# Kernel tuning notes

Hardware: AMD Instinct MI355X
Metric: run time of the kernel (lower is better)

Reference implementation:

```python
import jax, jax.numpy as jnp
import numpy as np
import math

D_MODEL = 1024
N_HEADS = 16
D_HEAD = 64
D_MLP = 4096
INIT_RANGE = 0.02
VAR_EPS = 1e-05
BATCH = 2
SEQ = 2048


def new_gelu(x):
    c = math.sqrt(2.0 / math.pi)
    return 0.5 * x * (1.0 + jnp.tanh(c * (x + 0.044715 * x ** 3)))


def layer_norm(x, w, b):
    mean = jnp.mean(x, axis=-1, keepdims=True)
    x = x - mean
    var = jnp.mean(x * x, axis=-1, keepdims=True)
    return x / jnp.sqrt(var + VAR_EPS) * w + b


def setup_inputs() -> dict:
    key = jax.random.key(0)
    ks = jax.random.split(key, 12)
    s = INIT_RANGE
    return {
        "resid": jax.random.normal(ks[0], (BATCH, SEQ, D_MODEL), jnp.float32),
        "w_q": s * jax.random.normal(ks[1], (N_HEADS, D_MODEL, D_HEAD), jnp.float32),
        "w_k": s * jax.random.normal(ks[2], (N_HEADS, D_MODEL, D_HEAD), jnp.float32),
        "w_v": s * jax.random.normal(ks[3], (N_HEADS, D_MODEL, D_HEAD), jnp.float32),
        "w_o": s * jax.random.normal(ks[4], (N_HEADS, D_HEAD, D_MODEL), jnp.float32),
        "ln1_w": s * jax.random.normal(ks[5], (D_MODEL,), jnp.float32),
        "ln1_b": jnp.zeros((D_MODEL,), jnp.float32),
        "ln2_w": s * jax.random.normal(ks[6], (D_MODEL,), jnp.float32),
        "ln2_b": jnp.zeros((D_MODEL,), jnp.float32),
        "w_in": s * jax.random.normal(ks[7], (D_MODEL, D_MLP), jnp.float32),
        "b_in": jnp.zeros((D_MLP,), jnp.float32),
        "w_out": s * jax.random.normal(ks[8], (D_MLP, D_MODEL), jnp.float32),
        "b_out": jnp.zeros((D_MODEL,), jnp.float32),
    }


def attention(x, w_q, w_k, w_v, w_o):
    # x: [b, s, d]; weights: [h, d, dh] / [h, dh, d]
    qs = jnp.einsum('bsd,hde->bhse', x, w_q)
    ks = jnp.einsum('bsd,hde->bhse', x, w_k)
    vs = jnp.einsum('bsd,hde->bhse', x, w_v)
    attn = jnp.einsum('bhqe,bhke->bhqk', qs, ks)  # [b, h, s, s]
    s = attn.shape[-1]
    causal = jnp.triu(jnp.ones((s, s), dtype=bool), k=1)
    attn = jnp.where(causal, -jnp.inf, attn)
    attn = jax.nn.softmax(attn / math.sqrt(D_HEAD), axis=-1)
    z = jnp.einsum('bhqk,bhke->bhqe', attn, vs)
    return jnp.einsum('bhse,hed->bsd', z, w_o)


def reference(resid, w_q, w_k, w_v, w_o, ln1_w, ln1_b, ln2_w, ln2_b, w_in, b_in, w_out, b_out):
    resid = resid + attention(layer_norm(resid, ln1_w, ln1_b), w_q, w_k, w_v, w_o)
    h = layer_norm(resid, ln2_w, ln2_b)
    h = new_gelu(jnp.einsum('bsd,dm->bsm', h, w_in) + b_in)
    resid = resid + jnp.einsum('bsm,md->bsd', h, w_out) + b_out
    return resid
```

## Files before the change

kernel.cpp:

```cpp
#include <hip/hip_runtime.h>

#define DEV static __device__ __forceinline__

typedef unsigned short u16;
typedef __attribute__((ext_vector_type(8))) __bf16 bf16x8;
typedef __attribute__((ext_vector_type(4))) float f32x4;

DEV float bf2f(u16 u) { union { unsigned int i; float f; } v; v.i = ((unsigned int)u) << 16; return v.f; }
DEV u16 f2bf(float f) {
  union { float f; unsigned int i; } v; v.f = f;
  unsigned int r = v.i + 0x7fffu + ((v.i >> 16) & 1u);
  return (u16)(r >> 16);
}

DEV float gelu_f(float x) {
  float u = 0.7978845608028654f * (x + 0.044715f * x * x * x);
  float e = __expf(2.f * u);
  float t = 1.f - 2.f / (e + 1.f);
  return 0.5f * x * (1.f + t);
}

DEV void async16(const u16* g, u16* l) {
  __builtin_amdgcn_global_load_lds(
      (const __attribute__((address_space(1))) unsigned int*)g,
      (__attribute__((address_space(3))) unsigned int*)l, 16, 0, 0);
}

__global__ __launch_bounds__(256) void transpose_conv(
    const float* __restrict__ in, u16* __restrict__ out, int R, int C,
    long inStride, long outStride)
{
  __shared__ float tile[32][33];
  const float* src = in + (size_t)blockIdx.z * inStride;
  u16* dst = out + (size_t)blockIdx.z * outStride;
  int c0 = blockIdx.x * 32, r0 = blockIdx.y * 32;
  int tx = threadIdx.x & 31, ty = threadIdx.x >> 5;
#pragma unroll
  for (int i = 0; i < 32; i += 8)
    tile[ty + i][tx] = src[(size_t)(r0 + ty + i) * C + (c0 + tx)];
  __syncthreads();
#pragma unroll
  for (int i = 0; i < 32; i += 8)
    dst[(size_t)(c0 + ty + i) * R + (r0 + tx)] = f2bf(tile[tx][ty + i]);
}

__global__ __launch_bounds__(256) void ln_kernel(
    const float* __restrict__ x, const float* __restrict__ g,
    const float* __restrict__ b, u16* __restrict__ out)
{
  int row = blockIdx.x, tid = threadIdx.x;
  const float4 v = ((const float4*)(x + (size_t)row * 1024))[tid];
  float s = v.x + v.y + v.z + v.w;
  float ss = v.x * v.x + v.y * v.y + v.z * v.z + v.w * v.w;
#pragma unroll
  for (int m = 1; m < 64; m <<= 1) { s += __shfl_xor(s, m, 64); ss += __shfl_xor(ss, m, 64); }
  __shared__ float red[8];
  if ((tid & 63) == 0) { red[tid >> 6] = s; red[4 + (tid >> 6)] = ss; }
  __syncthreads();
  s = red[0] + red[1] + red[2] + red[3];
  ss = red[4] + red[5] + red[6] + red[7];
  float mean = s * (1.f / 1024.f);
  float var = ss * (1.f / 1024.f) - mean * mean;
  float rstd = rsqrtf(var + 1e-5f);
  float4 gv = ((const float4*)g)[tid];
  float4 bv = ((const float4*)b)[tid];
  u16* o = out + (size_t)row * 1024 + tid * 4;
  o[0] = f2bf((v.x - mean) * rstd * gv.x + bv.x);
  o[1] = f2bf((v.y - mean) * rstd * gv.y + bv.y);
  o[2] = f2bf((v.z - mean) * rstd * gv.z + bv.z);
  o[3] = f2bf((v.w - mean) * rstd * gv.w + bv.w);
}

template <int EPI, int BM>
__global__ __launch_bounds__(256) void gemm_bf16(
    const u16* __restrict__ A, const u16* __restrict__ Bt, int K, int N,
    const float* __restrict__ addv, const float* __restrict__ bias,
    float* __restrict__ outF, u16* __restrict__ o0, u16* __restrict__ o1,
    u16* __restrict__ o2)
{
  constexpr int IT = BM / 32;
  __shared__ u16 lA[BM * 64];
  __shared__ u16 lB[128 * 64];
  const int tid = threadIdx.x;
  const int lane = tid & 63, wave = tid >> 6;
  const int wm = wave >> 1, wn = wave & 1;
  const int quad = lane >> 4, l16 = lane & 15;
  const int m0 = blockIdx.y * BM, n0 = blockIdx.x * 128;

  f32x4 acc[IT][4] = {};

  const int srow = lane >> 3;
  const int soff = ((lane & 7) ^ srow) << 3;

  for (int kt = 0; kt < K; kt += 64) {
    __syncthreads();
#pragma unroll
    for (int q = 0; q < BM / 32; ++q) {
      int rbase = wave * (BM / 4) + q * 8;
      async16(A + (size_t)(m0 + rbase + srow) * K + kt + soff, lA + rbase * 64);
    }
#pragma unroll
    for (int q = 0; q < 4; ++q) {
      int rbase = wave * 32 + q * 8;
      async16(Bt + (size_t)(n0 + rbase + srow) * K + kt + soff, lB + rbase * 64);
    }
    __syncthreads();
#pragma unroll
    for (int kk = 0; kk < 2; ++kk) {
      bf16x8 af[IT], bfr[4];
#pragma unroll
      for (int i = 0; i < IT; ++i) {
        int ar = wm * (BM / 2) + i * 16 + l16;
        af[i] = *(const bf16x8*)&lA[ar * 64 + ((((kk * 4) + quad) ^ (ar & 7)) << 3)];
      }
#pragma unroll
      for (int j = 0; j < 4; ++j) {
        int br = wn * 64 + j * 16 + l16;
        bfr[j] = *(const bf16x8*)&lB[br * 64 + ((((kk * 4) + quad) ^ (br & 7)) << 3)];
      }
#pragma unroll
      for (int i = 0; i < IT; ++i)
#pragma unroll
        for (int j = 0; j < 4; ++j)
          acc[i][j] = __builtin_amdgcn_mfma_f32_16x16x32_bf16(af[i], bfr[j], acc[i][j], 0, 0, 0);
    }
  }

#pragma unroll
  for (int i = 0; i < IT; ++i) {
    const int rowb = m0 + wm * (BM / 2) + i * 16 + quad * 4;
#pragma unroll
    for (int j = 0; j < 4; ++j) {
      const int col = n0 + wn * 64 + j * 16 + l16;
#pragma unroll
      for (int rr = 0; rr < 4; ++rr) {
        const int m = rowb + rr;
        const float v = acc[i][j][rr];
        if (EPI == 0) {
          int bb = m >> 11, s = m & 2047;
          int proj = col >> 10, hc = col & 1023, hh = hc >> 6, e = hc & 63;
          size_t bhh = (size_t)(bb * 16 + hh);
          if (proj == 0) o0[(bhh * 2048 + s) * 64 + e] = f2bf(v * 0.125f);
          else if (proj == 1) o1[(bhh * 2048 + s) * 64 + e] = f2bf(v);
          else o2[bhh * 131072 + (size_t)e * 2048 + s] = f2bf(v);
        } else if (EPI == 1) {
          size_t idx = (size_t)m * N + col;
          outF[idx] = v + addv[idx];
        } else if (EPI == 2) {
          o0[(size_t)m * N + col] = f2bf(gelu_f(v + bias[col]));
        } else {
          size_t idx = (size_t)m * N + col;
          outF[idx] = v + bias[col] + addv[idx];
        }
      }
    }
  }
}

__global__ __launch_bounds__(256) void attn_flash(
    const u16* __restrict__ Q, const u16* __restrict__ K,
    const u16* __restrict__ Vt, u16* __restrict__ Z)
{
  __shared__ u16 lK[64 * 64];
  __shared__ u16 lV[64 * 64];
  __shared__ u16 lP[4][16 * 64];

  const int tid = threadIdx.x;
  const int lane = tid & 63, wave = tid >> 6;
  const int quad = lane >> 4, l16 = lane & 15;

  const int flat = blockIdx.x;
  const int xcd = flat & 7, w = flat >> 3;
  const int bhid = xcd * 4 + (w >> 5);
  const int qtile = 31 - (w & 31);
  const int b = bhid >> 4, h = bhid & 15;
  const size_t bh = (size_t)bhid;
  const int q0b = qtile * 64;
  const int q0w = q0b + wave * 16;

  bf16x8 qf[2];
#pragma unroll
  for (int d = 0; d < 2; ++d)
    qf[d] = *(const bf16x8*)(Q + (bh * 2048 + (size_t)(q0w + l16)) * 64 + d * 32 + quad * 8);

  f32x4 oacc[4] = {};
  float lrow[4] = {};

  u16* myP = lP[wave];
  const int kend = q0b + 64;

  for (int kt0 = 0; kt0 < kend; kt0 += 64) {
    __syncthreads();
#pragma unroll
    for (int c = 0; c < 2; ++c) {
      int cl = tid + c * 256;
      int rrow = cl >> 3, ch = cl & 7;
      uint4 kv = *(const uint4*)(K + (bh * 2048 + (size_t)(kt0 + rrow)) * 64 + ch * 8);
      *(uint4*)(lK + rrow * 64 + ((ch ^ (rrow & 7)) << 3)) = kv;
      uint4 vv = *(const uint4*)(Vt + bh * 131072 + (size_t)rrow * 2048 + kt0 + ch * 8);
      *(uint4*)(lV + rrow * 64 + ((ch ^ (rrow & 7)) << 3)) = vv;
    }
    __syncthreads();

    bf16x8 kf[4][2];
#pragma unroll
    for (int j = 0; j < 4; ++j)
#pragma unroll
      for (int d = 0; d < 2; ++d) {
        int key = j * 16 + l16;
        kf[j][d] = *(const bf16x8*)(lK + key * 64 + (((d * 4 + quad) ^ (key & 7)) << 3));
      }
    f32x4 sv[4];
#pragma unroll
    for (int j = 0; j < 4; ++j) {
      f32x4 z = {};
      z = __builtin_amdgcn_mfma_f32_16x16x32_bf16(qf[0], kf[j][0], z, 0, 0, 0);
      z = __builtin_amdgcn_mfma_f32_16x16x32_bf16(qf[1], kf[j][1], z, 0, 0, 0);
      sv[j] = z;
    }

    const bool needMask = (kt0 + 63 > q0w);
#pragma unroll
    for (int rr = 0; rr < 4; ++rr) {
      int rowl = quad * 4 + rr;
      int rowg = q0w + rowl;
      u16* prow = myP + rowl * 64;
      float accl = lrow[rr];
#pragma unroll
      for (int j = 0; j < 4; ++j) {
        float p = __expf(sv[j][rr]);
        if (needMask && (kt0 + j * 16 + l16 > rowg)) p = 0.f;
        accl += p;
        int chk = j * 2 + (l16 >> 3);
        prow[((chk ^ (rowl & 7)) << 3) + (l16 & 7)] = (u16)(__float_as_uint(p) >> 16);
      }
      lrow[rr] = accl;
    }

#pragma unroll
    for (int ks = 0; ks < 2; ++ks) {
      int chk = ks * 4 + quad;
      bf16x8 pf, vf[4];
      pf = *(const bf16x8*)(myP + l16 * 64 + ((chk ^ (l16 & 7)) << 3));
#pragma unroll
      for (int d = 0; d < 4; ++d) {
        int dh = d * 16 + l16;
        vf[d] = *(const bf16x8*)(lV + dh * 64 + ((chk ^ (dh & 7)) << 3));
      }
#pragma unroll
      for (int d = 0; d < 4; ++d)
        oacc[d] = __builtin_amdgcn_mfma_f32_16x16x32_bf16(pf, vf[d], oacc[d], 0, 0, 0);
    }
  }

#pragma unroll
  for (int rr = 0; rr < 4; ++rr) {
    float l = lrow[rr];
#pragma unroll
    for (int msk = 1; msk < 16; msk <<= 1) l += __shfl_xor(l, msk, 64);
    lrow[rr] = 1.f / l;
  }
#pragma unroll
  for (int d = 0; d < 4; ++d)
#pragma unroll
    for (int rr = 0; rr < 4; ++rr) {
      int srow = q0w + quad * 4 + rr;
      Z[((size_t)(b * 2048 + srow)) * 1024 + h * 64 + d * 16 + l16] =
          f2bf(oacc[d][rr] * lrow[rr]);
    }
}

extern "C" void kernel_launch(void* const* d_in, const int* in_sizes, int n_in,
                              void* d_out, int out_size, void* d_ws, size_t ws_size,
                              hipStream_t stream) {
  const float* resid = (const float*)d_in[0];
  const float* w_q  = (const float*)d_in[1];
  const float* w_k  = (const float*)d_in[2];
  const float* w_v  = (const float*)d_in[3];
  const float* w_o  = (const float*)d_in[4];
  const float* ln1w = (const float*)d_in[5];
  const float* ln1b = (const float*)d_in[6];
  const float* ln2w = (const float*)d_in[7];
  const float* ln2b = (const float*)d_in[8];
  const float* w_in = (const float*)d_in[9];
  const float* b_in = (const float*)d_in[10];
  const float* w_out= (const float*)d_in[11];
  const float* b_out= (const float*)d_in[12];
  float* out = (float*)d_out;

  const size_t MB = 1u << 20;
  char* ws = (char*)d_ws;
  u16* WQKVT = (u16*)(ws + 0);
  u16* WOT   = (u16*)(ws + 6 * MB);
  u16* WINT  = (u16*)(ws + 8 * MB);
  u16* WOUTT = (u16*)(ws + 16 * MB);
  u16* X1    = (u16*)(ws + 24 * MB);
  u16* Qb    = (u16*)(ws + 32 * MB);
  u16* Kb    = (u16*)(ws + 40 * MB);
  u16* Vb    = (u16*)(ws + 48 * MB);
  u16* Zb    = (u16*)(ws + 56 * MB);
  float* R2  = (float*)(ws + 64 * MB);
  u16* Hb    = (u16*)(ws + 80 * MB);
  u16* Gb    = (u16*)(ws + 24 * MB);

  transpose_conv<<<dim3(2, 32, 16), 256, 0, stream>>>(w_q, WQKVT + 0 * 1024 * 1024, 1024, 64, 65536, 65536);
  transpose_conv<<<dim3(2, 32, 16), 256, 0, stream>>>(w_k, WQKVT + 1 * 1024 * 1024, 1024, 64, 65536, 65536);
  transpose_conv<<<dim3(2, 32, 16), 256, 0, stream>>>(w_v, WQKVT + 2 * 1024 * 1024, 1024, 64, 65536, 65536);
  transpose_conv<<<dim3(32, 32, 1), 256, 0, stream>>>(w_o, WOT, 1024, 1024, 0, 0);
  transpose_conv<<<dim3(128, 32, 1), 256, 0, stream>>>(w_in, WINT, 1024, 4096, 0, 0);
  transpose_conv<<<dim3(32, 128, 1), 256, 0, stream>>>(w_out, WOUTT, 4096, 1024, 0, 0);

  ln_kernel<<<4096, 256, 0, stream>>>(resid, ln1w, ln1b, X1);
  gemm_bf16<0, 128><<<dim3(24, 32), 256, 0, stream>>>(X1, WQKVT, 1024, 3072, nullptr, nullptr, nullptr, Qb, Kb, Vb);
  attn_flash<<<dim3(1024), 256, 0, stream>>>(Qb, Kb, Vb, Zb);
  gemm_bf16<1, 64><<<dim3(8, 64), 256, 0, stream>>>(Zb, WOT, 1024, 1024, resid, nullptr, R2, nullptr, nullptr, nullptr);
  ln_kernel<<<4096, 256, 0, stream>>>(R2, ln2w, ln2b, Hb);
  gemm_bf16<2, 128><<<dim3(32, 32), 256, 0, stream>>>(Hb, WINT, 1024, 4096, nullptr, b_in, nullptr, Gb, nullptr, nullptr);
  gemm_bf16<3, 64><<<dim3(8, 64), 256, 0, stream>>>(Gb, WOUTT, 4096, 1024, R2, b_out, out, nullptr, nullptr, nullptr);
}
```

Before: 374.5 us.

## Merge weight transposes, shrink GEMM tiles, async-load K/V in attention

Replaces the six weight transpose launches with a single kernel that dispatches by block index. The GEMM gains a BN template parameter, and every GEMM now uses smaller tiles (64x128 or 64x64), which gives more blocks to fill the CUs. The flash-attention K/V tile loads switch from register-staged copies to direct global-to-LDS async loads with the same swizzle. Smaller tiles reduce data reuse per block and raise global traffic in exchange for better occupancy and fewer launches.

Measured after the change: 372.5 us. No clear change (-0.5%).

```diff
diff --git a/kernel.cpp b/kernel.cpp
--- a/kernel.cpp
+++ b/kernel.cpp
@@ -26,14 +26,37 @@
       (__attribute__((address_space(3))) unsigned int*)l, 16, 0, 0);
 }
 
-__global__ __launch_bounds__(256) void transpose_conv(
-    const float* __restrict__ in, u16* __restrict__ out, int R, int C,
-    long inStride, long outStride)
+__global__ __launch_bounds__(256) void transpose_all(
+    const float* __restrict__ w_q, const float* __restrict__ w_k,
+    const float* __restrict__ w_v, const float* __restrict__ w_o,
+    const float* __restrict__ w_in, const float* __restrict__ w_out,
+    u16* __restrict__ WQKVT, u16* __restrict__ WOT,
+    u16* __restrict__ WINT, u16* __restrict__ WOUTT)
 {
+  int t = blockIdx.x;
+  const float* src; u16* dst; int R, C, c0, r0;
+  if (t < 3072) {
+    int seg = t >> 10, tt = t & 1023;
+    int z = tt >> 6, rem = tt & 63;
+    const float* w = seg == 0 ? w_q : (seg == 1 ? w_k : w_v);
+    src = w + z * 65536;
+    dst = WQKVT + seg * 1048576 + z * 65536;
+    R = 1024; C = 64;
+    c0 = (rem >> 5) * 32; r0 = (rem & 31) * 32;
+  } else if (t < 4096) {
+    int tt = t - 3072;
+    src = w_o; dst = WOT; R = 1024; C = 1024;
+    c0 = (tt & 31) * 32; r0 = (tt >> 5) * 32;
+  } else if (t < 8192) {
+    int tt = t - 4096;
+    src = w_in; dst = WINT; R = 1024; C = 4096;
+    c0 = (tt & 127) * 32; r0 = (tt >> 7) * 32;
+  } else {
+    int tt = t - 8192;
+    src = w_out; dst = WOUTT; R = 4096; C = 1024;
+    c0 = (tt & 31) * 32; r0 = (tt >> 5) * 32;
+  }
   __shared__ float tile[32][33];
-  const float* src = in + (size_t)blockIdx.z * inStride;
-  u16* dst = out + (size_t)blockIdx.z * outStride;
-  int c0 = blockIdx.x * 32, r0 = blockIdx.y * 32;
   int tx = threadIdx.x & 31, ty = threadIdx.x >> 5;
 #pragma unroll
   for (int i = 0; i < 32; i += 8)
@@ -71,23 +94,23 @@
   o[3] = f2bf((v.w - mean) * rstd * gv.w + bv.w);
 }
 
-template <int EPI, int BM>
+template <int EPI, int BM, int BN>
 __global__ __launch_bounds__(256) void gemm_bf16(
     const u16* __restrict__ A, const u16* __restrict__ Bt, int K, int N,
     const float* __restrict__ addv, const float* __restrict__ bias,
     float* __restrict__ outF, u16* __restrict__ o0, u16* __restrict__ o1,
     u16* __restrict__ o2)
 {
-  constexpr int IT = BM / 32;
+  constexpr int IM = BM / 32, IN = BN / 32;
   __shared__ u16 lA[BM * 64];
-  __shared__ u16 lB[128 * 64];
+  __shared__ u16 lB[BN * 64];
   const int tid = threadIdx.x;
   const int lane = tid & 63, wave = tid >> 6;
   const int wm = wave >> 1, wn = wave & 1;
   const int quad = lane >> 4, l16 = lane & 15;
-  const int m0 = blockIdx.y * BM, n0 = blockIdx.x * 128;
-
-  f32x4 acc[IT][4] = {};
+  const int m0 = blockIdx.y * BM, n0 = blockIdx.x * BN;
+
+  f32x4 acc[IM][IN] = {};
 
   const int srow = lane >> 3;
   const int soff = ((lane & 7) ^ srow) << 3;
@@ -100,38 +123,38 @@
       async16(A + (size_t)(m0 + rbase + srow) * K + kt + soff, lA + rbase * 64);
     }
 #pragma unroll
-    for (int q = 0; q < 4; ++q) {
-      int rbase = wave * 32 + q * 8;
+    for (int q = 0; q < BN / 32; ++q) {
+      int rbase = wave * (BN / 4) + q * 8;
       async16(Bt + (size_t)(n0 + rbase + srow) * K + kt + soff, lB + rbase * 64);
     }
     __syncthreads();
 #pragma unroll
     for (int kk = 0; kk < 2; ++kk) {
-      bf16x8 af[IT], bfr[4];
-#pragma unroll
-      for (int i = 0; i < IT; ++i) {
+      bf16x8 af[IM], bfr[IN];
+#pragma unroll
+      for (int i = 0; i < IM; ++i) {
         int ar = wm * (BM / 2) + i * 16 + l16;
         af[i] = *(const bf16x8*)&lA[ar * 64 + ((((kk * 4) + quad) ^ (ar & 7)) << 3)];
       }
 #pragma unroll
-      for (int j = 0; j < 4; ++j) {
-        int br = wn * 64 + j * 16 + l16;
+      for (int j = 0; j < IN; ++j) {
+        int br = wn * (BN / 2) + j * 16 + l16;
         bfr[j] = *(const bf16x8*)&lB[br * 64 + ((((kk * 4) + quad) ^ (br & 7)) << 3)];
       }
 #pragma unroll
-      for (int i = 0; i < IT; ++i)
-#pragma unroll
-        for (int j = 0; j < 4; ++j)
+      for (int i = 0; i < IM; ++i)
+#pragma unroll
+        for (int j = 0; j < IN; ++j)
           acc[i][j] = __builtin_amdgcn_mfma_f32_16x16x32_bf16(af[i], bfr[j], acc[i][j], 0, 0, 0);
     }
   }
 
 #pragma unroll
-  for (int i = 0; i < IT; ++i) {
+  for (int i = 0; i < IM; ++i) {
     const int rowb = m0 + wm * (BM / 2) + i * 16 + quad * 4;
 #pragma unroll
-    for (int j = 0; j < 4; ++j) {
-      const int col = n0 + wn * 64 + j * 16 + l16;
+    for (int j = 0; j < IN; ++j) {
+      const int col = n0 + wn * (BN / 2) + j * 16 + l16;
 #pragma unroll
       for (int rr = 0; rr < 4; ++rr) {
         const int m = rowb + rr;
@@ -178,6 +201,9 @@
   const int q0b = qtile * 64;
   const int q0w = q0b + wave * 16;
 
+  const int srow = lane >> 3;
+  const int soff = ((lane & 7) ^ srow) << 3;
+
   bf16x8 qf[2];
 #pragma unroll
   for (int d = 0; d < 2; ++d)
@@ -192,13 +218,10 @@
   for (int kt0 = 0; kt0 < kend; kt0 += 64) {
     __syncthreads();
 #pragma unroll
-    for (int c = 0; c < 2; ++c) {
-      int cl = tid + c * 256;
-      int rrow = cl >> 3, ch = cl & 7;
-      uint4 kv = *(const uint4*)(K + (bh * 2048 + (size_t)(kt0 + rrow)) * 64 + ch * 8);
-      *(uint4*)(lK + rrow * 64 + ((ch ^ (rrow & 7)) << 3)) = kv;
-      uint4 vv = *(const uint4*)(Vt + bh * 131072 + (size_t)rrow * 2048 + kt0 + ch * 8);
-      *(uint4*)(lV + rrow * 64 + ((ch ^ (rrow & 7)) << 3)) = vv;
+    for (int q = 0; q < 2; ++q) {
+      int rbase = wave * 16 + q * 8;
+      async16(K + (bh * 2048 + (size_t)(kt0 + rbase + srow)) * 64 + soff, lK + rbase * 64);
+      async16(Vt + bh * 131072 + (size_t)(rbase + srow) * 2048 + kt0 + soff, lV + rbase * 64);
     }
     __syncthreads();
 
@@ -264,8 +287,8 @@
   for (int d = 0; d < 4; ++d)
 #pragma unroll
     for (int rr = 0; rr < 4; ++rr) {
-      int srow = q0w + quad * 4 + rr;
-      Z[((size_t)(b * 2048 + srow)) * 1024 + h * 64 + d * 16 + l16] =
+      int srowq = q0w + quad * 4 + rr;
+      Z[((size_t)(b * 2048 + srowq)) * 1024 + h * 64 + d * 16 + l16] =
           f2bf(oacc[d][rr] * lrow[rr]);
     }
 }
@@ -303,18 +326,13 @@
   u16* Hb    = (u16*)(ws + 80 * MB);
   u16* Gb    = (u16*)(ws + 24 * MB);
 
-  transpose_conv<<<dim3(2, 32, 16), 256, 0, stream>>>(w_q, WQKVT + 0 * 1024 * 1024, 1024, 64, 65536, 65536);
-  transpose_conv<<<dim3(2, 32, 16), 256, 0, stream>>>(w_k, WQKVT + 1 * 1024 * 1024, 1024, 64, 65536, 65536);
-  transpose_conv<<<dim3(2, 32, 16), 256, 0, stream>>>(w_v, WQKVT + 2 * 1024 * 1024, 1024, 64, 65536, 65536);
-  transpose_conv<<<dim3(32, 32, 1), 256, 0, stream>>>(w_o, WOT, 1024, 1024, 0, 0);
-  transpose_conv<<<dim3(128, 32, 1), 256, 0, stream>>>(w_in, WINT, 1024, 4096, 0, 0);
-  transpose_conv<<<dim3(32, 128, 1), 256, 0, stream>>>(w_out, WOUTT, 4096, 1024, 0, 0);
-
+  transpose_all<<<dim3(12288), 256, 0, stream>>>(w_q, w_k, w_v, w_o, w_in, w_out,
+                                                 WQKVT, WOT, WINT, WOUTT);
   ln_kernel<<<4096, 256, 0, stream>>>(resid, ln1w, ln1b, X1);
-  gemm_bf16<0, 128><<<dim3(24, 32), 256, 0, stream>>>(X1, WQKVT, 1024, 3072, nullptr, nullptr, nullptr, Qb, Kb, Vb);
+  gemm_bf16<0, 64, 128><<<dim3(24, 64), 256, 0, stream>>>(X1, WQKVT, 1024, 3072, nullptr, nullptr, nullptr, Qb, Kb, Vb);
   attn_flash<<<dim3(1024), 256, 0, stream>>>(Qb, Kb, Vb, Zb);
-  gemm_bf16<1, 64><<<dim3(8, 64), 256, 0, stream>>>(Zb, WOT, 1024, 1024, resid, nullptr, R2, nullptr, nullptr, nullptr);
+  gemm_bf16<1, 64, 64><<<dim3(16, 64), 256, 0, stream>>>(Zb, WOT, 1024, 1024, resid, nullptr, R2, nullptr, nullptr, nullptr);
   ln_kernel<<<4096, 256, 0, stream>>>(R2, ln2w, ln2b, Hb);
-  gemm_bf16<2, 128><<<dim3(32, 32), 256, 0, stream>>>(Hb, WINT, 1024, 4096, nullptr, b_in, nullptr, Gb, nullptr, nullptr);
-  gemm_bf16<3, 64><<<dim3(8, 64), 256, 0, stream>>>(Gb, WOUTT, 4096, 1024, R2, b_out, out, nullptr, nullptr, nullptr);
-}
+  gemm_bf16<2, 64, 128><<<dim3(32, 64), 256, 0, stream>>>(Hb, WINT, 1024, 4096, nullptr, b_in, nullptr, Gb, nullptr, nullptr);
+  gemm_bf16<3, 64, 64><<<dim3(16, 64), 256, 0, stream>>>(Gb, WOUTT, 4096, 1024, R2, b_out, out, nullptr, nullptr, nullptr);
+}
```
